# Kernel tuning notes

Measured on AMD Instinct MI355X. Metric: run time of the kernel, lower is better.

The kernel has to match this reference:

```python
import jax, jax.numpy as jnp
import numpy as np

D_MODEL = 1024
D_STATE = 64
BATCH = 4
SEQ_L = 4096
LN_EPS = 1e-5


def setup_inputs() -> dict:
    key = jax.random.key(0)
    ks = jax.random.split(key, 8)
    u = jax.random.normal(ks[0], (BATCH, SEQ_L, D_MODEL), jnp.float32)
    # Parameters mirroring StateSpaceLayer._initialize_parameters
    A_log = jax.random.uniform(ks[1], (D_STATE,), jnp.float32, -2.0, -0.1)
    xav = float(np.sqrt(6.0 / (D_STATE + D_MODEL)))
    B = jax.random.uniform(ks[2], (D_STATE, D_MODEL), jnp.float32, -xav, xav) * 0.1
    C = jax.random.uniform(ks[3], (D_MODEL, D_STATE), jnp.float32, -xav, xav) * 0.1
    D = jnp.zeros((D_MODEL,), jnp.float32)
    delta = jax.random.uniform(ks[4], (D_MODEL,), jnp.float32, 0.001, 0.1)
    gamma = jnp.ones((D_MODEL,), jnp.float32)
    beta = jnp.zeros((D_MODEL,), jnp.float32)
    freq_align = jax.random.normal(ks[5], (D_MODEL,), jnp.float32)
    reward = jax.random.normal(ks[6], (D_MODEL,), jnp.float32)
    return dict(u=u, A_log=A_log, B=B, C=C, D=D, delta=delta,
                gamma=gamma, beta=beta, freq_align=freq_align, reward=reward)


def reference(u, A_log, B, C, D, delta, gamma, beta, freq_align, reward):
    b, L, d = u.shape
    A = -jnp.exp(A_log)                                   # [N]
    # --- convolution kernel: K[k] = C @ (A_bar[0])^k, A_bar[0] = exp(delta[0]*A) ---
    k_idx = jnp.arange(L, dtype=u.dtype)                  # [L]
    powers = jnp.exp(k_idx[:, None] * (delta[0] * A)[None, :])  # [L, N]
    K = jnp.einsum('ln,dn->ld', powers, C)                # [L, D]
    # --- FFT-based causal (circular, zero-padded) convolution ---
    fft_size = 1 << int(np.ceil(np.log2(2 * L)))
    u_fft = jnp.fft.fft(u, n=fft_size, axis=1)            # [B, F, D] complex
    K_fft = jnp.fft.fft(K, n=fft_size, axis=0)            # [F, D] complex
    y = jnp.fft.ifft(u_fft * K_fft[None], axis=1).real[:, :L, :]
    # --- D skip connection ---
    y = y + u * D
    # --- FFT-based learning signals: scale spectrum, add real 'reward' to every bin ---
    y_fft = jnp.fft.fft(y, axis=1)
    y = jnp.fft.ifft(y_fft * freq_align + reward, axis=1).real
    # --- LayerNorm (eval-mode dropout = identity) ---
    mean = y.mean(-1, keepdims=True)
    var = y.var(-1, keepdims=True)
    y = (y - mean) / jnp.sqrt(var + LN_EPS) * gamma + beta
    # --- final state update with mean timescale ---
    delta_mean = delta.mean()
    A_bar_s = jnp.exp(delta_mean * A)                     # [N]
    A_safe = A + 1e-8 * jnp.sign(A)
    B_bar = ((A_bar_s - 1.0) / A_safe)[:, None] * B       # [N, D]
    state = jnp.zeros((b, A.shape[0]), u.dtype)
    final_state = A_bar_s * state + jnp.einsum('nd,bd->bn', B_bar, u[:, -1, :])
    return (y, final_state)
```

## Files before the change

### kernel.cpp

```cpp
#include <hip/hip_runtime.h>
#include <math.h>

#define BATCH  4
#define SEQL   4096
#define DMODEL 1024
#define NSTATE 64
#define LN_EPS 1e-5f
#define TB     16

typedef unsigned short u16;
typedef float f32x2 __attribute__((ext_vector_type(2)));

__device__ __forceinline__ f32x2 fma2(f32x2 a, f32x2 b, f32x2 c) {
#if __has_builtin(__builtin_elementwise_fma)
    return __builtin_elementwise_fma(a, b, c);
#else
    f32x2 d; d.x = fmaf(a.x, b.x, c.x); d.y = fmaf(a.y, b.y, c.y); return d;
#endif
}

__device__ __forceinline__ u16 f2bf(float x) {
    unsigned int b = __float_as_uint(x);
    b += 0x7FFF + ((b >> 16) & 1);
    return (u16)(b >> 16);
}
__device__ __forceinline__ float bf2f(u16 h) {
    return __uint_as_float(((unsigned int)h) << 16);
}

__global__ __launch_bounds__(256) void k_local(const float* __restrict__ u,
                                               const float* __restrict__ A_log,
                                               const float* __restrict__ delta,
                                               u16* __restrict__ f,
                                               int NCH, int TCH) {
    __shared__ float r_lds[NSTATE];
    const int tid = threadIdx.x;
    const int w = tid >> 6, l = tid & 63;
    const int b   = blockIdx.x / (16 * NCH);
    const int rem = blockIdx.x % (16 * NCH);
    const int dt  = rem / NCH;
    const int j   = rem % NCH;
    const int n0  = w << 4;
    const int d   = (dt << 6) | l;

    if (tid < NSTATE) r_lds[tid] = expf(delta[0] * -expf(A_log[tid]));
    __syncthreads();

    f32x2 r2[8], s2[8];
#pragma unroll
    for (int p = 0; p < 8; ++p) {
        r2[p] = *(const f32x2*)&r_lds[n0 + 2 * p];
        s2[p] = (f32x2)(0.f, 0.f);
    }

    const float* ub = u + ((size_t)b * SEQL + (size_t)j * TCH) * DMODEL + d;
    for (int tb = 0; tb < TCH / TB; ++tb) {
        float ur[TB];
#pragma unroll
        for (int t = 0; t < TB; ++t)
            ur[t] = ub[(size_t)(tb * TB + t) * DMODEL];
#pragma unroll
        for (int q = 0; q < 4; ++q) {
            f32x2 sa = s2[2*q], sb = s2[2*q+1];
            const f32x2 ra = r2[2*q], rb = r2[2*q+1];
#pragma unroll
            for (int t = 0; t < TB; ++t) {
                f32x2 u2; u2.x = ur[t]; u2.y = ur[t];
                sa = fma2(ra, sa, u2);
                sb = fma2(rb, sb, u2);
            }
            s2[2*q] = sa; s2[2*q+1] = sb;
        }
    }
    u16* fb = f + (((size_t)b * NCH + j) * NSTATE + n0) * DMODEL + d;
#pragma unroll
    for (int p = 0; p < 8; ++p) {
        fb[(size_t)(2*p)     * DMODEL] = f2bf(s2[p].x);
        fb[(size_t)(2*p + 1) * DMODEL] = f2bf(s2[p].y);
    }
}

__global__ __launch_bounds__(256) void k_pass2(const float* __restrict__ A_log,
                                               const float* __restrict__ delta,
                                               u16* __restrict__ f,
                                               int NCH, int TCH) {
    const int tid = blockIdx.x * 256 + threadIdx.x;
    const int d = tid & (DMODEL - 1);
    const int n = (tid >> 10) & (NSTATE - 1);
    const int b = tid >> 16;
    const float A  = -expf(A_log[n]);
    const float rT = expf((float)TCH * delta[0] * A);
    float I = 0.f;
    u16* p = f + ((size_t)b * NCH * NSTATE + n) * DMODEL + d;
    const size_t stride = (size_t)NSTATE * DMODEL;
    for (int j = 0; j < NCH; ++j) {
        float tmp = bf2f(p[(size_t)j * stride]);
        p[(size_t)j * stride] = f2bf(I);
        I = fmaf(rT, I, tmp);
    }
}

template <bool ZBF16>
__global__ __launch_bounds__(256) void k_replay(const float* __restrict__ u,
                                                const float* __restrict__ A_log,
                                                const float* __restrict__ C,
                                                const float* __restrict__ Dvec,
                                                const float* __restrict__ delta,
                                                const u16* __restrict__ I,
                                                const float* __restrict__ fal,
                                                const float* __restrict__ rw,
                                                void* __restrict__ zout,
                                                int NCH, int TCH) {
    __shared__ float r_lds[NSTATE];
    __shared__ float part[2][4][TB][64];
    const int tid = threadIdx.x;
    const int w = tid >> 6, l = tid & 63;
    const int b   = blockIdx.x / (16 * NCH);
    const int rem = blockIdx.x % (16 * NCH);
    const int dt  = rem / NCH;
    const int j   = rem % NCH;
    const int n0  = w << 4;
    const int d   = (dt << 6) | l;

    if (tid < NSTATE) r_lds[tid] = expf(delta[0] * -expf(A_log[tid]));
    __syncthreads();

    const float fad = fal[d];
    f32x2 r2[8], c2[8], s2[8];
#pragma unroll
    for (int p = 0; p < 8; ++p)
        r2[p] = *(const f32x2*)&r_lds[n0 + 2 * p];
#pragma unroll
    for (int p = 0; p < 8; ++p) {
        c2[p].x = fad * C[(size_t)d * NSTATE + n0 + 2*p];
        c2[p].y = fad * C[(size_t)d * NSTATE + n0 + 2*p + 1];
    }
    const u16* Ib = I + (((size_t)b * NCH + j) * NSTATE + n0) * DMODEL + d;
#pragma unroll
    for (int p = 0; p < 8; ++p) {
        s2[p].x = bf2f(Ib[(size_t)(2*p)     * DMODEL]);
        s2[p].y = bf2f(Ib[(size_t)(2*p + 1) * DMODEL]);
    }

    const float Ddf = Dvec[d] * fad;
    const float rwd = rw[d];
    const float* ub = u + ((size_t)b * SEQL + (size_t)j * TCH) * DMODEL + d;
    const size_t zoff = ((size_t)b * SEQL + (size_t)j * TCH) * DMODEL + d;
    u16*   zb16 = (u16*)zout + zoff;
    float* zb32 = (float*)zout + zoff;

    for (int tb = 0; tb < TCH / TB; ++tb) {
        const int pb = tb & 1;
        float ur[TB];
        f32x2 zr2[TB];
#pragma unroll
        for (int t = 0; t < TB; ++t) {
            ur[t] = ub[(size_t)(tb * TB + t) * DMODEL];
            zr2[t] = (f32x2)(0.f, 0.f);
        }
#pragma unroll
        for (int q = 0; q < 4; ++q) {
            f32x2 sa = s2[2*q], sb = s2[2*q+1];
            const f32x2 ra = r2[2*q], rb = r2[2*q+1];
            const f32x2 ca = c2[2*q], cb = c2[2*q+1];
#pragma unroll
            for (int t = 0; t < TB; ++t) {
                f32x2 u2; u2.x = ur[t]; u2.y = ur[t];
                sa = fma2(ra, sa, u2);
                sb = fma2(rb, sb, u2);
                zr2[t] = fma2(ca, sa, zr2[t]);
                zr2[t] = fma2(cb, sb, zr2[t]);
            }
            s2[2*q] = sa; s2[2*q+1] = sb;
        }
#pragma unroll
        for (int t = 0; t < TB; ++t) {
            float v = zr2[t].x + zr2[t].y;
            if (w == 0) v = fmaf(Ddf, ur[t], v);
            part[pb][w][t][l] = v;
        }
        __syncthreads();
#pragma unroll
        for (int k = 0; k < 4; ++k) {
            const int t = (w << 2) | k;
            float v = (part[pb][0][t][l] + part[pb][1][t][l]) +
                      (part[pb][2][t][l] + part[pb][3][t][l]);
            if (j == 0 && tb == 0 && t == 0) v += rwd;
            if (ZBF16) zb16[(size_t)(tb * TB + t) * DMODEL] = f2bf(v);
            else       zb32[(size_t)(tb * TB + t) * DMODEL] = v;
        }
    }
}

template <bool ZBF16>
__global__ __launch_bounds__(256) void k_ln(const void* __restrict__ zin,
                                            float* __restrict__ y,
                                            const float* __restrict__ gamma,
                                            const float* __restrict__ beta) {
    const int tid = threadIdx.x;
    float4 v;
    if (ZBF16) {
        const ushort4 h = ((const ushort4*)((const u16*)zin + (size_t)blockIdx.x * DMODEL))[tid];
        v.x = bf2f(h.x); v.y = bf2f(h.y); v.z = bf2f(h.z); v.w = bf2f(h.w);
    } else {
        v = ((const float4*)((const float*)zin + (size_t)blockIdx.x * DMODEL))[tid];
    }
    float sum = v.x + v.y + v.z + v.w;
    float sq  = v.x*v.x + v.y*v.y + v.z*v.z + v.w*v.w;
#pragma unroll
    for (int off = 32; off > 0; off >>= 1) {
        sum += __shfl_down(sum, off, 64);
        sq  += __shfl_down(sq,  off, 64);
    }
    __shared__ float red[8];
    const int wave = tid >> 6, lane = tid & 63;
    if (lane == 0) { red[wave] = sum; red[4 + wave] = sq; }
    __syncthreads();
    sum = red[0] + red[1] + red[2] + red[3];
    sq  = red[4] + red[5] + red[6] + red[7];
    const float mean = sum * (1.f / DMODEL);
    const float var  = sq * (1.f / DMODEL) - mean * mean;
    const float inv  = 1.f / sqrtf(var + LN_EPS);
    const float4 g  = ((const float4*)gamma)[tid];
    const float4 bb = ((const float4*)beta)[tid];
    float4 o;
    o.x = (v.x - mean) * inv * g.x + bb.x;
    o.y = (v.y - mean) * inv * g.y + bb.y;
    o.z = (v.z - mean) * inv * g.z + bb.z;
    o.w = (v.w - mean) * inv * g.w + bb.w;
    ((float4*)(y + (size_t)blockIdx.x * DMODEL))[tid] = o;
}

__global__ __launch_bounds__(256) void k_state(const float* __restrict__ u,
                                               const float* __restrict__ A_log,
                                               const float* __restrict__ B,
                                               const float* __restrict__ delta,
                                               float* __restrict__ out) {
    const int n = blockIdx.x & 63;
    const int b = blockIdx.x >> 6;
    const int tid = threadIdx.x;
    const float* ul = u + ((size_t)b * SEQL + (SEQL - 1)) * DMODEL;
    const float* Bn = B + (size_t)n * DMODEL;
    float dot = 0.f, dsum = 0.f;
    for (int dd = tid; dd < DMODEL; dd += 256) {
        dot = fmaf(Bn[dd], ul[dd], dot);
        dsum += delta[dd];
    }
#pragma unroll
    for (int off = 32; off > 0; off >>= 1) {
        dot  += __shfl_down(dot,  off, 64);
        dsum += __shfl_down(dsum, off, 64);
    }
    __shared__ float red[8];
    const int wave = tid >> 6, lane = tid & 63;
    if (lane == 0) { red[wave] = dot; red[4 + wave] = dsum; }
    __syncthreads();
    if (tid == 0) {
        dot  = red[0] + red[1] + red[2] + red[3];
        dsum = red[4] + red[5] + red[6] + red[7];
        const float dmean = dsum * (1.f / DMODEL);
        const float A = -expf(A_log[n]);
        const float Abar = expf(dmean * A);
        const float Asafe = A + (A >= 0.f ? 1e-8f : -1e-8f);
        out[blockIdx.x] = ((Abar - 1.f) / Asafe) * dot;
    }
}

extern "C" void kernel_launch(void* const* d_in, const int* in_sizes, int n_in,
                              void* d_out, int out_size, void* d_ws, size_t ws_size,
                              hipStream_t stream) {
    const float* u     = (const float*)d_in[0];
    const float* A_log = (const float*)d_in[1];
    const float* B     = (const float*)d_in[2];
    const float* C     = (const float*)d_in[3];
    const float* Dv    = (const float*)d_in[4];
    const float* delta = (const float*)d_in[5];
    const float* gamma = (const float*)d_in[6];
    const float* beta  = (const float*)d_in[7];
    const float* fal   = (const float*)d_in[8];
    const float* rw    = (const float*)d_in[9];

    float* y  = (float*)d_out;
    float* st = y + (size_t)BATCH * SEQL * DMODEL;
    u16* f    = (u16*)d_ws;

    int NCH = 32;
    while (NCH > 4 && (size_t)BATCH * NCH * NSTATE * DMODEL * sizeof(u16) > ws_size)
        NCH >>= 1;
    const int TCH = SEQL / NCH;
    const int nb = BATCH * 16 * NCH;

    const size_t f_bytes = (size_t)BATCH * NCH * NSTATE * DMODEL * sizeof(u16);
    const size_t z_bytes = (size_t)BATCH * SEQL * DMODEL * sizeof(u16);
    const bool zbf16 = (f_bytes + z_bytes) <= ws_size;
    void* zbuf = zbf16 ? (void*)((char*)d_ws + f_bytes) : (void*)y;

    hipLaunchKernelGGL(k_local, dim3(nb), dim3(256), 0, stream, u, A_log, delta, f, NCH, TCH);
    hipLaunchKernelGGL(k_pass2, dim3(BATCH * NSTATE * DMODEL / 256), dim3(256), 0, stream,
                       A_log, delta, f, NCH, TCH);
    if (zbf16) {
        hipLaunchKernelGGL((k_replay<true>), dim3(nb), dim3(256), 0, stream,
                           u, A_log, C, Dv, delta, f, fal, rw, zbuf, NCH, TCH);
        hipLaunchKernelGGL((k_ln<true>), dim3(BATCH * SEQL), dim3(256), 0, stream,
                           zbuf, y, gamma, beta);
    } else {
        hipLaunchKernelGGL((k_replay<false>), dim3(nb), dim3(256), 0, stream,
                           u, A_log, C, Dv, delta, f, fal, rw, zbuf, NCH, TCH);
        hipLaunchKernelGGL((k_ln<false>), dim3(BATCH * SEQL), dim3(256), 0, stream,
                           zbuf, y, gamma, beta);
    }
    hipLaunchKernelGGL(k_state, dim3(BATCH * NSTATE), dim3(256), 0, stream,
                       u, A_log, B, delta, st);
}
```

Before: 124.1 us.

## Process two model channels per thread with vector loads in scan kernels

Each thread in k_local and k_replay now owns two adjacent d channels and 16 states, loading u as float2 and packing bf16 state/output pairs into 32-bit stores. This halves the block count and widens memory accesses. The packed-FMA lanes now carry two channels instead of two states, which removes the broadcast of u. The replay time block shrinks from 16 to 8 steps to limit register pressure from the larger per-thread state, at the cost of more barriers per chunk and possibly lower occupancy.

```diff
diff --git a/kernel.cpp b/kernel.cpp
--- a/kernel.cpp
+++ b/kernel.cpp
@@ -6,9 +6,11 @@
 #define DMODEL 1024
 #define NSTATE 64
 #define LN_EPS 1e-5f
-#define TB     16
+#define TB     8
+#define TBL    16
 
 typedef unsigned short u16;
+typedef unsigned int   u32;
 typedef float f32x2 __attribute__((ext_vector_type(2)));
 
 __device__ __forceinline__ f32x2 fma2(f32x2 a, f32x2 b, f32x2 c) {
@@ -20,12 +22,18 @@
 }
 
 __device__ __forceinline__ u16 f2bf(float x) {
-    unsigned int b = __float_as_uint(x);
+    u32 b = __float_as_uint(x);
     b += 0x7FFF + ((b >> 16) & 1);
     return (u16)(b >> 16);
 }
 __device__ __forceinline__ float bf2f(u16 h) {
-    return __uint_as_float(((unsigned int)h) << 16);
+    return __uint_as_float(((u32)h) << 16);
+}
+__device__ __forceinline__ u32 pack2bf(f32x2 v) {
+    return (u32)f2bf(v.x) | ((u32)f2bf(v.y) << 16);
+}
+__device__ __forceinline__ f32x2 unpack2bf(u32 p) {
+    f32x2 v; v.x = bf2f((u16)p); v.y = bf2f((u16)(p >> 16)); return v;
 }
 
 __global__ __launch_bounds__(256) void k_local(const float* __restrict__ u,
@@ -36,48 +44,49 @@
     __shared__ float r_lds[NSTATE];
     const int tid = threadIdx.x;
     const int w = tid >> 6, l = tid & 63;
-    const int b   = blockIdx.x / (16 * NCH);
-    const int rem = blockIdx.x % (16 * NCH);
+    const int b   = blockIdx.x / (8 * NCH);
+    const int rem = blockIdx.x % (8 * NCH);
     const int dt  = rem / NCH;
     const int j   = rem % NCH;
     const int n0  = w << 4;
-    const int d   = (dt << 6) | l;
+    const int d0  = (dt << 7) | (l << 1);
 
     if (tid < NSTATE) r_lds[tid] = expf(delta[0] * -expf(A_log[tid]));
     __syncthreads();
 
-    f32x2 r2[8], s2[8];
-#pragma unroll
-    for (int p = 0; p < 8; ++p) {
-        r2[p] = *(const f32x2*)&r_lds[n0 + 2 * p];
-        s2[p] = (f32x2)(0.f, 0.f);
-    }
-
-    const float* ub = u + ((size_t)b * SEQL + (size_t)j * TCH) * DMODEL + d;
-    for (int tb = 0; tb < TCH / TB; ++tb) {
-        float ur[TB];
-#pragma unroll
-        for (int t = 0; t < TB; ++t)
-            ur[t] = ub[(size_t)(tb * TB + t) * DMODEL];
+    f32x2 r2[16], s2[16];
+#pragma unroll
+    for (int i = 0; i < 16; ++i) {
+        const float rn = r_lds[n0 + i];
+        r2[i].x = rn; r2[i].y = rn;
+        s2[i] = (f32x2)(0.f, 0.f);
+    }
+
+    const float* ub = u + ((size_t)b * SEQL + (size_t)j * TCH) * DMODEL + d0;
+    for (int tb = 0; tb < TCH / TBL; ++tb) {
+        f32x2 ur[TBL];
+#pragma unroll
+        for (int t = 0; t < TBL; ++t)
+            ur[t] = *(const f32x2*)&ub[(size_t)(tb * TBL + t) * DMODEL];
 #pragma unroll
         for (int q = 0; q < 4; ++q) {
-            f32x2 sa = s2[2*q], sb = s2[2*q+1];
-            const f32x2 ra = r2[2*q], rb = r2[2*q+1];
-#pragma unroll
-            for (int t = 0; t < TB; ++t) {
-                f32x2 u2; u2.x = ur[t]; u2.y = ur[t];
+            f32x2 sa = s2[4*q], sb = s2[4*q+1], sc = s2[4*q+2], sd = s2[4*q+3];
+            const f32x2 ra = r2[4*q], rb = r2[4*q+1], rc = r2[4*q+2], rd = r2[4*q+3];
+#pragma unroll
+            for (int t = 0; t < TBL; ++t) {
+                const f32x2 u2 = ur[t];
                 sa = fma2(ra, sa, u2);
                 sb = fma2(rb, sb, u2);
+                sc = fma2(rc, sc, u2);
+                sd = fma2(rd, sd, u2);
             }
-            s2[2*q] = sa; s2[2*q+1] = sb;
-        }
-    }
-    u16* fb = f + (((size_t)b * NCH + j) * NSTATE + n0) * DMODEL + d;
-#pragma unroll
-    for (int p = 0; p < 8; ++p) {
-        fb[(size_t)(2*p)     * DMODEL] = f2bf(s2[p].x);
-        fb[(size_t)(2*p + 1) * DMODEL] = f2bf(s2[p].y);
-    }
+            s2[4*q] = sa; s2[4*q+1] = sb; s2[4*q+2] = sc; s2[4*q+3] = sd;
+        }
+    }
+    u32* fb = (u32*)(f + (((size_t)b * NCH + j) * NSTATE + n0) * DMODEL + d0);
+#pragma unroll
+    for (int i = 0; i < 16; ++i)
+        fb[(size_t)i * (DMODEL / 2)] = pack2bf(s2[i]);
 }
 
 __global__ __launch_bounds__(256) void k_pass2(const float* __restrict__ A_log,
@@ -112,82 +121,85 @@
                                                 void* __restrict__ zout,
                                                 int NCH, int TCH) {
     __shared__ float r_lds[NSTATE];
-    __shared__ float part[2][4][TB][64];
+    __shared__ f32x2 part[2][4][TB][64];
     const int tid = threadIdx.x;
     const int w = tid >> 6, l = tid & 63;
-    const int b   = blockIdx.x / (16 * NCH);
-    const int rem = blockIdx.x % (16 * NCH);
+    const int b   = blockIdx.x / (8 * NCH);
+    const int rem = blockIdx.x % (8 * NCH);
     const int dt  = rem / NCH;
     const int j   = rem % NCH;
     const int n0  = w << 4;
-    const int d   = (dt << 6) | l;
+    const int d0  = (dt << 7) | (l << 1);
 
     if (tid < NSTATE) r_lds[tid] = expf(delta[0] * -expf(A_log[tid]));
     __syncthreads();
 
-    const float fad = fal[d];
-    f32x2 r2[8], c2[8], s2[8];
-#pragma unroll
-    for (int p = 0; p < 8; ++p)
-        r2[p] = *(const f32x2*)&r_lds[n0 + 2 * p];
-#pragma unroll
-    for (int p = 0; p < 8; ++p) {
-        c2[p].x = fad * C[(size_t)d * NSTATE + n0 + 2*p];
-        c2[p].y = fad * C[(size_t)d * NSTATE + n0 + 2*p + 1];
-    }
-    const u16* Ib = I + (((size_t)b * NCH + j) * NSTATE + n0) * DMODEL + d;
-#pragma unroll
-    for (int p = 0; p < 8; ++p) {
-        s2[p].x = bf2f(Ib[(size_t)(2*p)     * DMODEL]);
-        s2[p].y = bf2f(Ib[(size_t)(2*p + 1) * DMODEL]);
-    }
-
-    const float Ddf = Dvec[d] * fad;
-    const float rwd = rw[d];
-    const float* ub = u + ((size_t)b * SEQL + (size_t)j * TCH) * DMODEL + d;
-    const size_t zoff = ((size_t)b * SEQL + (size_t)j * TCH) * DMODEL + d;
-    u16*   zb16 = (u16*)zout + zoff;
+    const float fa0 = fal[d0], fa1 = fal[d0 + 1];
+    f32x2 r2[16], c2[16], s2[16];
+#pragma unroll
+    for (int i = 0; i < 16; ++i) {
+        const float rn = r_lds[n0 + i];
+        r2[i].x = rn; r2[i].y = rn;
+        c2[i].x = fa0 * C[(size_t)d0       * NSTATE + n0 + i];
+        c2[i].y = fa1 * C[(size_t)(d0 + 1) * NSTATE + n0 + i];
+    }
+    const u32* Ib = (const u32*)(I + (((size_t)b * NCH + j) * NSTATE + n0) * DMODEL + d0);
+#pragma unroll
+    for (int i = 0; i < 16; ++i)
+        s2[i] = unpack2bf(Ib[(size_t)i * (DMODEL / 2)]);
+
+    f32x2 Ddf2; Ddf2.x = Dvec[d0] * fa0; Ddf2.y = Dvec[d0 + 1] * fa1;
+    f32x2 rw2;  rw2.x  = rw[d0];         rw2.y  = rw[d0 + 1];
+    const float* ub = u + ((size_t)b * SEQL + (size_t)j * TCH) * DMODEL + d0;
+    const size_t zoff = ((size_t)b * SEQL + (size_t)j * TCH) * DMODEL + d0;
+    u32*   zb16 = (u32*)((u16*)zout + zoff);
     float* zb32 = (float*)zout + zoff;
 
     for (int tb = 0; tb < TCH / TB; ++tb) {
         const int pb = tb & 1;
-        float ur[TB];
-        f32x2 zr2[TB];
+        f32x2 ur[TB], zr[TB];
 #pragma unroll
         for (int t = 0; t < TB; ++t) {
-            ur[t] = ub[(size_t)(tb * TB + t) * DMODEL];
-            zr2[t] = (f32x2)(0.f, 0.f);
+            ur[t] = *(const f32x2*)&ub[(size_t)(tb * TB + t) * DMODEL];
+            zr[t] = (f32x2)(0.f, 0.f);
         }
 #pragma unroll
         for (int q = 0; q < 4; ++q) {
-            f32x2 sa = s2[2*q], sb = s2[2*q+1];
-            const f32x2 ra = r2[2*q], rb = r2[2*q+1];
-            const f32x2 ca = c2[2*q], cb = c2[2*q+1];
+            f32x2 sa = s2[4*q], sb = s2[4*q+1], sc = s2[4*q+2], sd = s2[4*q+3];
+            const f32x2 ra = r2[4*q], rb = r2[4*q+1], rc = r2[4*q+2], rd = r2[4*q+3];
+            const f32x2 ca = c2[4*q], cb = c2[4*q+1], cc = c2[4*q+2], cd = c2[4*q+3];
 #pragma unroll
             for (int t = 0; t < TB; ++t) {
-                f32x2 u2; u2.x = ur[t]; u2.y = ur[t];
+                const f32x2 u2 = ur[t];
                 sa = fma2(ra, sa, u2);
                 sb = fma2(rb, sb, u2);
-                zr2[t] = fma2(ca, sa, zr2[t]);
-                zr2[t] = fma2(cb, sb, zr2[t]);
+                sc = fma2(rc, sc, u2);
+                sd = fma2(rd, sd, u2);
+                f32x2 a = fma2(ca, sa, zr[t]);
+                a = fma2(cb, sb, a);
+                a = fma2(cc, sc, a);
+                zr[t] = fma2(cd, sd, a);
             }
-            s2[2*q] = sa; s2[2*q+1] = sb;
+            s2[4*q] = sa; s2[4*q+1] = sb; s2[4*q+2] = sc; s2[4*q+3] = sd;
         }
 #pragma unroll
         for (int t = 0; t < TB; ++t) {
-            float v = zr2[t].x + zr2[t].y;
-            if (w == 0) v = fmaf(Ddf, ur[t], v);
+            f32x2 v = zr[t];
+            if (w == 0) v = fma2(Ddf2, ur[t], v);
             part[pb][w][t][l] = v;
         }
         __syncthreads();
 #pragma unroll
-        for (int k = 0; k < 4; ++k) {
-            const int t = (w << 2) | k;
-            float v = (part[pb][0][t][l] + part[pb][1][t][l]) +
-                      (part[pb][2][t][l] + part[pb][3][t][l]);
-            if (j == 0 && tb == 0 && t == 0) v += rwd;
-            if (ZBF16) zb16[(size_t)(tb * TB + t) * DMODEL] = f2bf(v);
-            else       zb32[(size_t)(tb * TB + t) * DMODEL] = v;
+        for (int k = 0; k < 2; ++k) {
+            const int t = (w << 1) | k;
+            f32x2 v;
+            v.x = (part[pb][0][t][l].x + part[pb][1][t][l].x) +
+                  (part[pb][2][t][l].x + part[pb][3][t][l].x);
+            v.y = (part[pb][0][t][l].y + part[pb][1][t][l].y) +
+                  (part[pb][2][t][l].y + part[pb][3][t][l].y);
+            if (j == 0 && tb == 0 && t == 0) { v.x += rw2.x; v.y += rw2.y; }
+            if (ZBF16) zb16[((size_t)(tb * TB + t) * DMODEL) / 2] = pack2bf(v);
+            else       *(f32x2*)&zb32[(size_t)(tb * TB + t) * DMODEL] = v;
         }
     }
 }
@@ -288,7 +300,7 @@
     while (NCH > 4 && (size_t)BATCH * NCH * NSTATE * DMODEL * sizeof(u16) > ws_size)
         NCH >>= 1;
     const int TCH = SEQL / NCH;
-    const int nb = BATCH * 16 * NCH;
+    const int nb = BATCH * 8 * NCH;
 
     const size_t f_bytes = (size_t)BATCH * NCH * NSTATE * DMODEL * sizeof(u16);
     const size_t z_bytes = (size_t)BATCH * SEQL * DMODEL * sizeof(u16);
```

New measurement: 132.4 us. 1.07x slower.
